# Optimization experiments

Hardware: AMD Instinct MI355X
Metric: run time of the kernel (lower is better)

The kernel has to match this reference:

```python
import jax, jax.numpy as jnp
import numpy as np

SPECIES = (0, 1)
CUTOFF = 6.0
N_ATOMS, N_EDGES, N_TRIPLETS = 20000, 500000, 2000000

G2_ETAS = np.array([0.003214, 0.035711, 0.071421, 0.124987, 0.214264, 0.357106, 0.714213, 1.428426], dtype=np.float32)
G4_ETAS = np.array([0.000357, 0.028569, 0.089277], dtype=np.float32)
G4_ZETAS = np.array([1.0, 2.0, 4.0], dtype=np.float32)
G4_LMDAS = np.array([-1.0, 1.0], dtype=np.float32)


def setup_inputs() -> dict:
    key = jax.random.key(0)
    ks = jax.random.split(key, 6)
    atomic_numbers = jax.random.randint(ks[0], (N_ATOMS,), 0, 2, dtype=jnp.int32)
    edge_index = jax.random.randint(ks[1], (2, N_EDGES), 0, N_ATOMS, dtype=jnp.int32)
    D_st = jax.random.uniform(ks[2], (N_EDGES,), minval=0.5, maxval=6.5, dtype=jnp.float32)
    id3_ba = jax.random.randint(ks[3], (N_TRIPLETS,), 0, N_EDGES, dtype=jnp.int32)
    id3_ca = jax.random.randint(ks[4], (N_TRIPLETS,), 0, N_EDGES, dtype=jnp.int32)
    cosphi = jax.random.uniform(ks[5], (N_TRIPLETS,), minval=-1.0, maxval=1.0, dtype=jnp.float32)
    # per-key parameters: 4 ordered species pairs for G2, 6 species triples for G4
    g2_etas = jnp.tile(jnp.asarray(G2_ETAS), (4, 1))
    g4_etas = jnp.tile(jnp.asarray(G4_ETAS), (6, 1))
    g4_zetas = jnp.tile(jnp.asarray(G4_ZETAS), (6, 1))
    g4_lmdas = jnp.tile(jnp.asarray(G4_LMDAS), (6, 1))
    return {"atomic_numbers": atomic_numbers, "edge_index": edge_index, "D_st": D_st,
            "id3_ba": id3_ba, "id3_ca": id3_ca, "cosphi": cosphi,
            "g2_etas": g2_etas, "g4_etas": g4_etas, "g4_zetas": g4_zetas, "g4_lmdas": g4_lmdas}


def _fc(R):
    # cosine cutoff (no in-range bool here; G4 applies its own range masks)
    return 0.5 * jnp.cos(jnp.pi * R / CUTOFF) + 0.5


def _acsf(atomic_numbers, edge_index, D_st, id3_ba, id3_ca, cosphi,
          g2_etas, g4_etas, g4_zetas, g4_lmdas):
    N = atomic_numbers.shape[0]
    dt = D_st.dtype
    src, tgt = edge_index[0], edge_index[1]
    an_src, an_tgt = atomic_numbers[src], atomic_numbers[tgt]

    # ---- triplet geometry (masking replaces boolean gather; scatter-add is equivalent) ----
    m3 = id3_ba > id3_ca                       # [T] triplet dedup mask
    R_ba = D_st[id3_ba]                        # [T]
    R_ca = D_st[id3_ca]
    sb = atomic_numbers[src[id3_ba]]           # species of edge-ba source
    tb = atomic_numbers[tgt[id3_ba]]           # species of central atom a
    sc = atomic_numbers[src[id3_ca]]
    seg3 = tgt[id3_ba]                         # scatter target: central atom index
    Rbc2 = R_ba * R_ba + R_ca * R_ca - 2.0 * R_ba * R_ca * cosphi
    R_bc = jnp.sqrt(jnp.maximum(Rbc2, 1e-12))
    in_range = ((R_bc < CUTOFF) & (R_ba < CUTOFF) & (R_ca < CUTOFF)).astype(dt)
    cut3 = _fc(R_ca) * _fc(R_bc) * _fc(R_ba) * in_range   # [T]
    r2sum = R_bc * R_bc + R_ba * R_ba + R_ca * R_ca       # [T]

    # ---- G2: per (source, target) species pair ----
    cut2 = _fc(D_st)                           # [E]
    d2 = D_st * D_st
    g2_per = {}
    k = 0
    for a1 in SPECIES:
        for a2 in SPECIES:
            w = ((an_tgt == a2) & (an_src == a1)).astype(dt)       # [E]
            res = (cut2 * w)[:, None] * jnp.exp(-g2_etas[k][None, :] * d2[:, None])  # [E,8]
            g2_per[(a1, a2)] = jax.ops.segment_sum(res, tgt, num_segments=N)        # [N,8]
            k += 1

    # ---- G4: per (a, b, c) species triple (b<=c) ----
    ns = len(SPECIES)
    g4_per = {}
    k = 0
    for a in SPECIES:
        for i in range(ns):
            b = SPECIES[i]
            for j in range(i, ns):
                c = SPECIES[j]
                idx = (((sb == b) & (tb == a) & (sc == c)) |
                       ((sb == c) & (tb == a) & (sc == b)))
                w = (m3 & idx).astype(dt)                                  # [T]
                eta, zta, lmda = g4_etas[k], g4_zetas[k], g4_lmdas[k]
                rad = jnp.exp(-eta[None, :] * r2sum[:, None])              # [T,3]
                cl = jnp.abs(1.0 + lmda[None, :, None] * cosphi[:, None, None]) ** zta[None, None, :]  # [T,2,3]
                res = cl[:, None, :, :] * rad[:, :, None, None] * (cut3 * w)[:, None, None, None]      # [T,3,2,3]
                g4 = jax.ops.segment_sum(res, seg3, num_segments=N)        # [N,3,2,3]
                g4_per[(a, b, c)] = (2.0 ** (1.0 - zta))[None, None, None, :] * g4
                k += 1

    # ---- assemble per-atom descriptor [N, 70]; rows carry their species' descriptor ----
    outs = []
    for a in SPECIES:
        mask = (atomic_numbers == a).astype(dt)[:, None]
        g2s = jnp.stack([g2_per[(s, a)] for s in SPECIES], axis=-1).reshape(N, -1)   # [N,16]
        trips = [(b, c) for i, b in enumerate(SPECIES) for c in SPECIES[i:]]
        g4s = jnp.stack([g4_per[(a, b, c)] for (b, c) in trips], axis=-1).reshape(N, -1)  # [N,54]
        outs.append(mask * jnp.concatenate([g2s, g4s], axis=-1))
    return outs[0] + outs[1]


def reference(atomic_numbers, edge_index, D_st, id3_ba, id3_ca, cosphi,
              g2_etas, g4_etas, g4_zetas, g4_lmdas):
    return _acsf(atomic_numbers, edge_index, D_st, id3_ba, id3_ca, cosphi,
                 g2_etas, g4_etas, g4_zetas, g4_lmdas)
```

## Files before the change

kernel.cpp:

```cpp
#include <hip/hip_runtime.h>


#define CAP_T 96
#define CAP_E 64

static __device__ __forceinline__ float fc_dev(float R) {
    const float PI_OVER_CUT = 0.52359877559829887308f;
    return fmaf(0.5f, __cosf(PI_OVER_CUT * R), 0.5f);
}


__global__ void edges_bin_kernel(const int* __restrict__ an,
                                 const int* __restrict__ ei,
                                 const float* __restrict__ D,
                                 const float* __restrict__ g2_etas,
                                 uint2* __restrict__ epack,
                                 int* __restrict__ ecount,
                                 float2* __restrict__ erec,
                                 float* __restrict__ out, int E) {
    int e = blockIdx.x * blockDim.x + threadIdx.x;
    if (e >= E) return;
    float d = D[e];
    int src = ei[e];
    int tgt = ei[E + e];
    int as = an[src];
    epack[e] = make_uint2(__float_as_uint(d), ((unsigned)tgt << 1) | (unsigned)as);
    float fcv = fc_dev(d);
    float d2 = d * d;
    int slot = atomicAdd(&ecount[tgt], 1);
    if (slot < CAP_E) {
        unsigned fp = (__float_as_uint(fcv) & ~1u) | (unsigned)as;
        erec[(size_t)tgt * CAP_E + slot] = make_float2(__uint_as_float(fp), d2);
    } else {
        int at = an[tgt];
        const float* eta = g2_etas + (as * 2 + at) * 8;
        float* row = out + (size_t)tgt * 70 + as;
#pragma unroll
        for (int i = 0; i < 8; ++i)
            atomicAdd(row + 2 * i, fcv * __expf(-eta[i] * d2));
    }
}

static __device__ __forceinline__ void process_triplet(
        int eba, int eca, float cph,
        const uint2* __restrict__ epack,
        const int* __restrict__ an,
        const float* __restrict__ g4_etas,
        const float* __restrict__ g4_zetas,
        const float* __restrict__ g4_lmdas,
        int* __restrict__ tcount, float4* __restrict__ trec,
        float* __restrict__ out) {
    if (eba <= eca) return;
    uint2 pb = epack[eba];
    uint2 pc = epack[eca];
    float R_ba = __uint_as_float(pb.x);
    float R_ca = __uint_as_float(pc.x);
    if (R_ba >= 6.0f || R_ca >= 6.0f) return;
    float Rbc2 = R_ba * R_ba + R_ca * R_ca - 2.0f * R_ba * R_ca * cph;
    float Rm2 = fmaxf(Rbc2, 1e-12f);
    float R_bc = sqrtf(Rm2);
    if (R_bc >= 6.0f) return;
    int seg = (int)(pb.y >> 1);
    int trip = (int)(pb.y & 1u) + (int)(pc.y & 1u);
    float cut3 = fc_dev(R_ba) * fc_dev(R_ca) * fc_dev(R_bc);
    float r2sum = Rm2 + R_ba * R_ba + R_ca * R_ca;
    float lg0 = __log2f(fabsf(fmaf(-1.0f, cph, 1.0f)));
    float lg1 = __log2f(fabsf(fmaf(+1.0f, cph, 1.0f)));
    int slot = atomicAdd(&tcount[seg], 1);
    if (slot < CAP_T) {
        unsigned cu = (__float_as_uint(cut3) & ~3u) | (unsigned)trip;
        trec[(size_t)seg * CAP_T + slot] =
            make_float4(__uint_as_float(cu), r2sum, lg0, lg1);
    } else {
        int A = an[seg];
        int k4 = A * 3 + trip;
        const float* eta = g4_etas + k4 * 3;
        const float* zet = g4_zetas + k4 * 3;
        const float* lmd = g4_lmdas + k4 * 2;
        float rad[3];
#pragma unroll
        for (int e2 = 0; e2 < 3; ++e2)
            rad[e2] = __expf(-eta[e2] * r2sum) * cut3;
        float l0 = (lmd[0] < 0.0f) ? lg0 : lg1;
        float l1 = (lmd[1] < 0.0f) ? lg0 : lg1;
        float* row = out + (size_t)seg * 70 + 16 + trip;
#pragma unroll
        for (int z = 0; z < 3; ++z) {
            float zv = zet[z], base = 1.0f - zv;
            float c0 = exp2f(fmaf(zv, l0, base));
            float c1 = exp2f(fmaf(zv, l1, base));
#pragma unroll
            for (int e2 = 0; e2 < 3; ++e2) {
                atomicAdd(row + ((e2 * 2 + 0) * 3 + z) * 3, c0 * rad[e2]);
                atomicAdd(row + ((e2 * 2 + 1) * 3 + z) * 3, c1 * rad[e2]);
            }
        }
    }
}

__global__ void trip_bin_kernel(const uint2* __restrict__ epack,
                                const int* __restrict__ id3_ba,
                                const int* __restrict__ id3_ca,
                                const float* __restrict__ cosphi,
                                const int* __restrict__ an,
                                const float* __restrict__ g4_etas,
                                const float* __restrict__ g4_zetas,
                                const float* __restrict__ g4_lmdas,
                                int* __restrict__ tcount,
                                float4* __restrict__ trec,
                                float* __restrict__ out, int T) {
    int i = blockIdx.x * blockDim.x + threadIdx.x;
    int t0 = i * 2;
    if (t0 >= T) return;
    if (t0 + 1 < T) {
        int2   ba = ((const int2*)id3_ba)[i];
        int2   ca = ((const int2*)id3_ca)[i];
        float2 cp = ((const float2*)cosphi)[i];
        process_triplet(ba.x, ca.x, cp.x, epack, an, g4_etas, g4_zetas,
                        g4_lmdas, tcount, trec, out);
        process_triplet(ba.y, ca.y, cp.y, epack, an, g4_etas, g4_zetas,
                        g4_lmdas, tcount, trec, out);
    } else {
        process_triplet(id3_ba[t0], id3_ca[t0], cosphi[t0], epack, an,
                        g4_etas, g4_zetas, g4_lmdas, tcount, trec, out);
    }
}

__global__ __launch_bounds__(256) void gather_kernel(
        const int* __restrict__ an,
        const float* __restrict__ g2_etas,
        const float* __restrict__ g4_etas,
        const float* __restrict__ g4_zetas,
        const float* __restrict__ g4_lmdas,
        const int* __restrict__ tcount, const float4* __restrict__ trec,
        const int* __restrict__ ecount, const float2* __restrict__ erec,
        float* __restrict__ out, int N) {
    __shared__ float4 sg4[4][64];
    __shared__ float2 sg2[4][64];
    int w = threadIdx.x >> 6;
    int lane = threadIdx.x & 63;
    int a = blockIdx.x * 4 + w;
    if (a >= N) return;
    int A = an[a];

    int trip_c = lane % 3;
    int z_c = (lane / 3) % 3;
    int l_c = (lane / 9) % 2;
    int e_c = lane / 18;
    float eta = 0.f, zv = 0.f, base = 1.f;
    if (lane < 54) {
        int k4 = A * 3 + trip_c;
        eta = g4_etas[k4 * 3 + e_c];
        zv  = g4_zetas[k4 * 3 + z_c];
        float lm = g4_lmdas[k4 * 2 + l_c];
        l_c = (lm < 0.0f) ? 0 : 1;
        base = 1.0f - zv;
    }
    int n_t = min(tcount[a], CAP_T);
    const float4* rec = trec + (size_t)a * CAP_T;
    float acc = 0.0f;
    for (int b0 = 0; b0 < n_t; b0 += 64) {
        int nch = min(64, n_t - b0);
        if (lane < nch) sg4[w][lane] = rec[b0 + lane];
        for (int i = 0; i < nch; ++i) {
            float4 b = sg4[w][i];
            unsigned cu = __float_as_uint(b.x);
            int btr = (int)(cu & 3u);
            float bc = __uint_as_float(cu & ~3u);
            float radv = __expf(-eta * b.y);
            float lg = l_c ? b.w : b.z;
            float cl = exp2f(fmaf(zv, lg, base));
            acc += (btr == trip_c) ? cl * radv * bc : 0.0f;
        }
    }
    if (lane < 54) out[(size_t)a * 70 + 16 + lane] += acc;

    int s_c = lane & 1;
    int i_c = lane >> 1;
    float eta2 = (lane < 16) ? g2_etas[(s_c * 2 + A) * 8 + i_c] : 0.0f;
    int n_e = min(ecount[a], CAP_E);
    const float2* erc = erec + (size_t)a * CAP_E;
    float acc2 = 0.0f;
    for (int b0 = 0; b0 < n_e; b0 += 64) {
        int nch = min(64, n_e - b0);
        if (lane < nch) sg2[w][lane] = erc[b0 + lane];
        for (int i = 0; i < nch; ++i) {
            float2 b = sg2[w][i];
            unsigned fp = __float_as_uint(b.x);
            int sp = (int)(fp & 1u);
            float fcv = __uint_as_float(fp & ~1u);
            float v = fcv * __expf(-eta2 * b.y);
            acc2 += (sp == s_c) ? v : 0.0f;
        }
    }
    if (lane < 16) out[(size_t)a * 70 + lane] += acc2;
}


__global__ void acsf_edges_kernel(const int* __restrict__ an,
                                  const int* __restrict__ ei,
                                  const float* __restrict__ D,
                                  const float* __restrict__ g2_etas,
                                  float2* __restrict__ edata,
                                  float* __restrict__ out,
                                  int E, int use_ws) {
    int e = blockIdx.x * blockDim.x + threadIdx.x;
    if (e >= E) return;
    float d = D[e];
    float cut2 = fc_dev(d);
    if (use_ws) edata[e] = make_float2(d, cut2);
    int src = ei[e];
    int tgt = ei[E + e];
    int as = an[src];
    int at = an[tgt];
    float d2 = d * d;
    const float* eta = g2_etas + (as * 2 + at) * 8;
    float* row = out + (size_t)tgt * 70 + as;
#pragma unroll
    for (int i = 0; i < 8; ++i)
        atomicAdd(row + 2 * i, cut2 * __expf(-eta[i] * d2));
}

__global__ void acsf_triplets_kernel(const int* __restrict__ an,
                                     const int* __restrict__ ei,
                                     const float* __restrict__ D,
                                     const float2* __restrict__ edata,
                                     const int* __restrict__ id3_ba,
                                     const int* __restrict__ id3_ca,
                                     const float* __restrict__ cosphi,
                                     const float* __restrict__ g4_etas,
                                     const float* __restrict__ g4_zetas,
                                     const float* __restrict__ g4_lmdas,
                                     float* __restrict__ out,
                                     int T, int E, int use_ws) {
    int t = blockIdx.x * blockDim.x + threadIdx.x;
    if (t >= T) return;
    int eba = id3_ba[t];
    int eca = id3_ca[t];
    if (eba <= eca) return;
    float R_ba, R_ca, fba, fca;
    if (use_ws) {
        float2 va = edata[eba];
        float2 vb = edata[eca];
        R_ba = va.x; fba = va.y;
        R_ca = vb.x; fca = vb.y;
    } else {
        R_ba = D[eba]; R_ca = D[eca];
        fba = fc_dev(R_ba); fca = fc_dev(R_ca);
    }
    if (R_ba >= 6.0f || R_ca >= 6.0f) return;
    float cph = cosphi[t];
    float Rbc2 = R_ba * R_ba + R_ca * R_ca - 2.0f * R_ba * R_ca * cph;
    float Rm2 = fmaxf(Rbc2, 1e-12f);
    float R_bc = sqrtf(Rm2);
    if (R_bc >= 6.0f) return;
    int seg = ei[E + eba];
    int A = an[seg];
    int sb = an[ei[eba]];
    int sc = an[ei[eca]];
    int trip = sb + sc;
    int k4 = A * 3 + trip;
    float cut3 = fba * fca * fc_dev(R_bc);
    float r2sum = Rm2 + R_ba * R_ba + R_ca * R_ca;
    const float* eta = g4_etas + k4 * 3;
    const float* zet = g4_zetas + k4 * 3;
    const float* lmd = g4_lmdas + k4 * 2;
    float rad[3];
#pragma unroll
    for (int e2 = 0; e2 < 3; ++e2)
        rad[e2] = __expf(-eta[e2] * r2sum) * cut3;
    float lg0 = __log2f(fabsf(fmaf(lmd[0], cph, 1.0f)));
    float lg1 = __log2f(fabsf(fmaf(lmd[1], cph, 1.0f)));
    float* row = out + (size_t)seg * 70 + 16 + trip;
#pragma unroll
    for (int z = 0; z < 3; ++z) {
        float zv = zet[z], bse = 1.0f - zv;
        float c0 = exp2f(fmaf(zv, lg0, bse));
        float c1 = exp2f(fmaf(zv, lg1, bse));
#pragma unroll
        for (int e2 = 0; e2 < 3; ++e2) {
            atomicAdd(row + ((e2 * 2 + 0) * 3 + z) * 3, c0 * rad[e2]);
            atomicAdd(row + ((e2 * 2 + 1) * 3 + z) * 3, c1 * rad[e2]);
        }
    }
}


extern "C" void kernel_launch(void* const* d_in, const int* in_sizes, int n_in,
                              void* d_out, int out_size, void* d_ws, size_t ws_size,
                              hipStream_t stream) {
    const int*   an       = (const int*)d_in[0];
    const int*   ei       = (const int*)d_in[1];
    const float* D        = (const float*)d_in[2];
    const int*   id3_ba   = (const int*)d_in[3];
    const int*   id3_ca   = (const int*)d_in[4];
    const float* cosphi   = (const float*)d_in[5];
    const float* g2_etas  = (const float*)d_in[6];
    const float* g4_etas  = (const float*)d_in[7];
    const float* g4_zetas = (const float*)d_in[8];
    const float* g4_lmdas = (const float*)d_in[9];
    (void)n_in;

    int N = in_sizes[0];
    int E = in_sizes[2];
    int T = in_sizes[3];
    float* out = (float*)d_out;

    size_t trec_b  = (size_t)N * CAP_T * sizeof(float4);
    size_t epack_b = (size_t)E * sizeof(uint2);
    size_t erec_b  = (size_t)N * CAP_E * sizeof(float2);
    size_t cnt_b   = (size_t)N * sizeof(int) * 2;
    size_t need = trec_b + epack_b + erec_b + cnt_b;

    const int blk = 256;
    hipMemsetAsync(d_out, 0, (size_t)out_size * sizeof(float), stream);

    if (ws_size >= need) {
        char* p = (char*)d_ws;
        float4* trec  = (float4*)p;            p += trec_b;
        uint2*  epack = (uint2*)p;             p += epack_b;
        float2* erec  = (float2*)p;            p += erec_b;
        int*    tcount = (int*)p;
        int*    ecount = tcount + N;
        hipMemsetAsync(tcount, 0, cnt_b, stream);

        edges_bin_kernel<<<(E + blk - 1) / blk, blk, 0, stream>>>(
            an, ei, D, g2_etas, epack, ecount, erec, out, E);
        int tthreads = (T + 1) / 2;
        trip_bin_kernel<<<(tthreads + blk - 1) / blk, blk, 0, stream>>>(
            epack, id3_ba, id3_ca, cosphi, an,
            g4_etas, g4_zetas, g4_lmdas, tcount, trec, out, T);
        gather_kernel<<<(N + 3) / 4, blk, 0, stream>>>(
            an, g2_etas, g4_etas, g4_zetas, g4_lmdas,
            tcount, trec, ecount, erec, out, N);
    } else {
        int use_ws = (ws_size >= (size_t)E * sizeof(float2)) ? 1 : 0;
        float2* edata = (float2*)d_ws;
        acsf_edges_kernel<<<(E + blk - 1) / blk, blk, 0, stream>>>(
            an, ei, D, g2_etas, edata, out, E, use_ws);
        acsf_triplets_kernel<<<(T + blk - 1) / blk, blk, 0, stream>>>(
            an, ei, D, edata, id3_ba, id3_ca, cosphi,
            g4_etas, g4_zetas, g4_lmdas, out, T, E, use_ws);
    }
}
```

Measured before the change: 196.1 us.

## Quantize edge and triplet records to shrink intermediate traffic

Edge data is packed into one 32-bit word (a 16-bit quantized distance, the target index and the source species), and triplet records shrink from float4 to float2 by quantizing cosphi and the cutoff product. The gather kernel now recomputes the log terms and fc from the decoded values. Triplet and edge binning each handle more items per thread with vector nontemporal loads. This cuts memory traffic and atomic-bin storage, but adds quantization error, extra transcendental work in the gather, and a limit of N <= 32767.

```diff
diff --git a/kernel.cpp b/kernel.cpp
--- a/kernel.cpp
+++ b/kernel.cpp
@@ -3,74 +3,99 @@
 
 #define CAP_T 96
 #define CAP_E 64
+
+typedef int    vi2 __attribute__((ext_vector_type(2)));
+typedef int    vi4 __attribute__((ext_vector_type(4)));
+typedef float  vf2 __attribute__((ext_vector_type(2)));
+typedef float  vf4 __attribute__((ext_vector_type(4)));
 
 static __device__ __forceinline__ float fc_dev(float R) {
     const float PI_OVER_CUT = 0.52359877559829887308f;
     return fmaf(0.5f, __cosf(PI_OVER_CUT * R), 0.5f);
 }
 
+static __device__ __forceinline__ unsigned enc_R(float d) {
+    float u = rintf(d * (65535.0f / 8.0f));
+    u = fminf(fmaxf(u, 0.0f), 65535.0f);
+    return (unsigned)u;
+}
+static __device__ __forceinline__ float dec_R(unsigned pk) {
+    return (float)(pk >> 16) * (8.0f / 65535.0f);
+}
+
+
+static __device__ __forceinline__ void process_edge(
+        int e, float d, int src, int tgt,
+        const int* __restrict__ an, const float* __restrict__ g2_etas,
+        unsigned* __restrict__ epack, int* __restrict__ ecount,
+        unsigned* __restrict__ erec, float* __restrict__ out) {
+    int as = an[src];
+    unsigned pk = (enc_R(d) << 16) | ((unsigned)tgt << 1) | (unsigned)as;
+    epack[e] = pk;
+    int slot = atomicAdd(&ecount[tgt], 1);
+    if (slot < CAP_E) {
+        erec[(size_t)tgt * CAP_E + slot] = pk;
+    } else {
+        float fcv = fc_dev(d), d2 = d * d;
+        int at = an[tgt];
+        const float* eta = g2_etas + (as * 2 + at) * 8;
+        float* row = out + (size_t)tgt * 70 + as;
+#pragma unroll
+        for (int i = 0; i < 8; ++i)
+            atomicAdd(row + 2 * i, fcv * __expf(-eta[i] * d2));
+    }
+}
 
 __global__ void edges_bin_kernel(const int* __restrict__ an,
                                  const int* __restrict__ ei,
                                  const float* __restrict__ D,
                                  const float* __restrict__ g2_etas,
-                                 uint2* __restrict__ epack,
+                                 unsigned* __restrict__ epack,
                                  int* __restrict__ ecount,
-                                 float2* __restrict__ erec,
+                                 unsigned* __restrict__ erec,
                                  float* __restrict__ out, int E) {
-    int e = blockIdx.x * blockDim.x + threadIdx.x;
-    if (e >= E) return;
-    float d = D[e];
-    int src = ei[e];
-    int tgt = ei[E + e];
-    int as = an[src];
-    epack[e] = make_uint2(__float_as_uint(d), ((unsigned)tgt << 1) | (unsigned)as);
-    float fcv = fc_dev(d);
-    float d2 = d * d;
-    int slot = atomicAdd(&ecount[tgt], 1);
-    if (slot < CAP_E) {
-        unsigned fp = (__float_as_uint(fcv) & ~1u) | (unsigned)as;
-        erec[(size_t)tgt * CAP_E + slot] = make_float2(__uint_as_float(fp), d2);
-    } else {
-        int at = an[tgt];
-        const float* eta = g2_etas + (as * 2 + at) * 8;
-        float* row = out + (size_t)tgt * 70 + as;
-#pragma unroll
-        for (int i = 0; i < 8; ++i)
-            atomicAdd(row + 2 * i, fcv * __expf(-eta[i] * d2));
+    int i = blockIdx.x * blockDim.x + threadIdx.x;
+    int e0 = i * 2;
+    if (e0 >= E) return;
+    if (e0 + 1 < E) {
+        vi2 sp = __builtin_nontemporal_load((const vi2*)ei + i);
+        vi2 tp = __builtin_nontemporal_load((const vi2*)(ei + E) + i);
+        vf2 dp = __builtin_nontemporal_load((const vf2*)D + i);
+        process_edge(e0,     dp.x, sp.x, tp.x, an, g2_etas, epack, ecount, erec, out);
+        process_edge(e0 + 1, dp.y, sp.y, tp.y, an, g2_etas, epack, ecount, erec, out);
+    } else {
+        process_edge(e0, D[e0], ei[e0], ei[E + e0], an, g2_etas, epack, ecount,
+                     erec, out);
     }
 }
 
 static __device__ __forceinline__ void process_triplet(
-        int eba, int eca, float cph,
-        const uint2* __restrict__ epack,
+        unsigned pb, unsigned pc, float cph,
         const int* __restrict__ an,
         const float* __restrict__ g4_etas,
         const float* __restrict__ g4_zetas,
         const float* __restrict__ g4_lmdas,
-        int* __restrict__ tcount, float4* __restrict__ trec,
+        int* __restrict__ tcount, vf2* __restrict__ trec,
         float* __restrict__ out) {
-    if (eba <= eca) return;
-    uint2 pb = epack[eba];
-    uint2 pc = epack[eca];
-    float R_ba = __uint_as_float(pb.x);
-    float R_ca = __uint_as_float(pc.x);
+    float R_ba = dec_R(pb);
+    float R_ca = dec_R(pc);
     if (R_ba >= 6.0f || R_ca >= 6.0f) return;
     float Rbc2 = R_ba * R_ba + R_ca * R_ca - 2.0f * R_ba * R_ca * cph;
     float Rm2 = fmaxf(Rbc2, 1e-12f);
     float R_bc = sqrtf(Rm2);
     if (R_bc >= 6.0f) return;
-    int seg = (int)(pb.y >> 1);
-    int trip = (int)(pb.y & 1u) + (int)(pc.y & 1u);
+    int seg = (int)((pb >> 1) & 0x7FFFu);
+    int trip = (int)(pb & 1u) + (int)(pc & 1u);
     float cut3 = fc_dev(R_ba) * fc_dev(R_ca) * fc_dev(R_bc);
     float r2sum = Rm2 + R_ba * R_ba + R_ca * R_ca;
-    float lg0 = __log2f(fabsf(fmaf(-1.0f, cph, 1.0f)));
-    float lg1 = __log2f(fabsf(fmaf(+1.0f, cph, 1.0f)));
     int slot = atomicAdd(&tcount[seg], 1);
     if (slot < CAP_T) {
-        unsigned cu = (__float_as_uint(cut3) & ~3u) | (unsigned)trip;
-        trec[(size_t)seg * CAP_T + slot] =
-            make_float4(__uint_as_float(cu), r2sum, lg0, lg1);
+        float cqf = fminf(fmaxf(fmaf(cph, 32767.5f, 32767.5f), 0.0f), 65535.0f);
+        unsigned cq = (unsigned)rintf(cqf);
+        unsigned c3q = (unsigned)rintf(cut3 * 16383.0f);
+        unsigned w0 = (cq << 16) | (c3q << 2) | (unsigned)trip;
+        vf2 r; r.x = __uint_as_float(w0); r.y = r2sum;
+        trec[(size_t)seg * CAP_T + slot] = r;
     } else {
         int A = an[seg];
         int k4 = A * 3 + trip;
@@ -81,14 +106,14 @@
 #pragma unroll
         for (int e2 = 0; e2 < 3; ++e2)
             rad[e2] = __expf(-eta[e2] * r2sum) * cut3;
-        float l0 = (lmd[0] < 0.0f) ? lg0 : lg1;
-        float l1 = (lmd[1] < 0.0f) ? lg0 : lg1;
+        float lg0 = __log2f(fabsf(fmaf(lmd[0], cph, 1.0f)));
+        float lg1 = __log2f(fabsf(fmaf(lmd[1], cph, 1.0f)));
         float* row = out + (size_t)seg * 70 + 16 + trip;
 #pragma unroll
         for (int z = 0; z < 3; ++z) {
             float zv = zet[z], base = 1.0f - zv;
-            float c0 = exp2f(fmaf(zv, l0, base));
-            float c1 = exp2f(fmaf(zv, l1, base));
+            float c0 = exp2f(fmaf(zv, lg0, base));
+            float c1 = exp2f(fmaf(zv, lg1, base));
 #pragma unroll
             for (int e2 = 0; e2 < 3; ++e2) {
                 atomicAdd(row + ((e2 * 2 + 0) * 3 + z) * 3, c0 * rad[e2]);
@@ -98,7 +123,7 @@
     }
 }
 
-__global__ void trip_bin_kernel(const uint2* __restrict__ epack,
+__global__ void trip_bin_kernel(const unsigned* __restrict__ epack,
                                 const int* __restrict__ id3_ba,
                                 const int* __restrict__ id3_ca,
                                 const float* __restrict__ cosphi,
@@ -107,22 +132,45 @@
                                 const float* __restrict__ g4_zetas,
                                 const float* __restrict__ g4_lmdas,
                                 int* __restrict__ tcount,
-                                float4* __restrict__ trec,
+                                vf2* __restrict__ trec,
                                 float* __restrict__ out, int T) {
     int i = blockIdx.x * blockDim.x + threadIdx.x;
-    int t0 = i * 2;
+    int t0 = i * 4;
     if (t0 >= T) return;
-    if (t0 + 1 < T) {
-        int2   ba = ((const int2*)id3_ba)[i];
-        int2   ca = ((const int2*)id3_ca)[i];
-        float2 cp = ((const float2*)cosphi)[i];
-        process_triplet(ba.x, ca.x, cp.x, epack, an, g4_etas, g4_zetas,
-                        g4_lmdas, tcount, trec, out);
-        process_triplet(ba.y, ca.y, cp.y, epack, an, g4_etas, g4_zetas,
-                        g4_lmdas, tcount, trec, out);
-    } else {
-        process_triplet(id3_ba[t0], id3_ca[t0], cosphi[t0], epack, an,
-                        g4_etas, g4_zetas, g4_lmdas, tcount, trec, out);
+    int ba[4], ca[4];
+    float cp[4];
+    if (t0 + 3 < T) {
+        vi4 b4 = __builtin_nontemporal_load((const vi4*)id3_ba + i);
+        vi4 c4 = __builtin_nontemporal_load((const vi4*)id3_ca + i);
+        vf4 p4 = __builtin_nontemporal_load((const vf4*)cosphi + i);
+        ba[0] = b4.x; ba[1] = b4.y; ba[2] = b4.z; ba[3] = b4.w;
+        ca[0] = c4.x; ca[1] = c4.y; ca[2] = c4.z; ca[3] = c4.w;
+        cp[0] = p4.x; cp[1] = p4.y; cp[2] = p4.z; cp[3] = p4.w;
+    } else {
+#pragma unroll
+        for (int k = 0; k < 4; ++k) {
+            int t = t0 + k;
+            ba[k] = (t < T) ? id3_ba[t] : 0;
+            ca[k] = (t < T) ? id3_ca[t] : 0;
+            cp[k] = (t < T) ? cosphi[t] : 0.0f;
+        }
+    }
+    unsigned pb[4], pc[4];
+    bool m[4];
+#pragma unroll
+    for (int k = 0; k < 4; ++k) {
+        m[k] = ba[k] > ca[k];
+        pb[k] = 0u; pc[k] = 0u;
+        if (m[k]) {
+            pb[k] = epack[ba[k]];
+            pc[k] = epack[ca[k]];
+        }
+    }
+#pragma unroll
+    for (int k = 0; k < 4; ++k) {
+        if (m[k])
+            process_triplet(pb[k], pc[k], cp[k], an, g4_etas, g4_zetas,
+                            g4_lmdas, tcount, trec, out);
     }
 }
 
@@ -132,11 +180,11 @@
         const float* __restrict__ g4_etas,
         const float* __restrict__ g4_zetas,
         const float* __restrict__ g4_lmdas,
-        const int* __restrict__ tcount, const float4* __restrict__ trec,
-        const int* __restrict__ ecount, const float2* __restrict__ erec,
+        const int* __restrict__ tcount, const vf2* __restrict__ trec,
+        const int* __restrict__ ecount, const unsigned* __restrict__ erec,
         float* __restrict__ out, int N) {
-    __shared__ float4 sg4[4][64];
-    __shared__ float2 sg2[4][64];
+    __shared__ vf2      sg4[4][64];
+    __shared__ unsigned sg2[4][64];
     int w = threadIdx.x >> 6;
     int lane = threadIdx.x & 63;
     int a = blockIdx.x * 4 + w;
@@ -147,30 +195,30 @@
     int z_c = (lane / 3) % 3;
     int l_c = (lane / 9) % 2;
     int e_c = lane / 18;
-    float eta = 0.f, zv = 0.f, base = 1.f;
+    float eta = 0.f, zv = 0.f, lm = 0.f, base = 1.f;
     if (lane < 54) {
         int k4 = A * 3 + trip_c;
         eta = g4_etas[k4 * 3 + e_c];
         zv  = g4_zetas[k4 * 3 + z_c];
-        float lm = g4_lmdas[k4 * 2 + l_c];
-        l_c = (lm < 0.0f) ? 0 : 1;
+        lm  = g4_lmdas[k4 * 2 + l_c];
         base = 1.0f - zv;
     }
     int n_t = min(tcount[a], CAP_T);
-    const float4* rec = trec + (size_t)a * CAP_T;
+    const vf2* rec = trec + (size_t)a * CAP_T;
     float acc = 0.0f;
     for (int b0 = 0; b0 < n_t; b0 += 64) {
         int nch = min(64, n_t - b0);
-        if (lane < nch) sg4[w][lane] = rec[b0 + lane];
+        if (lane < nch) sg4[w][lane] = __builtin_nontemporal_load(rec + b0 + lane);
         for (int i = 0; i < nch; ++i) {
-            float4 b = sg4[w][i];
-            unsigned cu = __float_as_uint(b.x);
-            int btr = (int)(cu & 3u);
-            float bc = __uint_as_float(cu & ~3u);
+            vf2 b = sg4[w][i];
+            unsigned w0 = __float_as_uint(b.x);
+            int btr = (int)(w0 & 3u);
+            float cut3 = (float)((w0 >> 2) & 0x3FFFu) * (1.0f / 16383.0f);
+            float c = fmaf((float)(w0 >> 16), 2.0f / 65535.0f, -1.0f);
             float radv = __expf(-eta * b.y);
-            float lg = l_c ? b.w : b.z;
-            float cl = exp2f(fmaf(zv, lg, base));
-            acc += (btr == trip_c) ? cl * radv * bc : 0.0f;
+            float al = fabsf(fmaf(lm, c, 1.0f));
+            float cl = exp2f(fmaf(zv, __log2f(al), base));
+            acc += (btr == trip_c) ? cl * radv * cut3 : 0.0f;
         }
     }
     if (lane < 54) out[(size_t)a * 70 + 16 + lane] += acc;
@@ -179,17 +227,16 @@
     int i_c = lane >> 1;
     float eta2 = (lane < 16) ? g2_etas[(s_c * 2 + A) * 8 + i_c] : 0.0f;
     int n_e = min(ecount[a], CAP_E);
-    const float2* erc = erec + (size_t)a * CAP_E;
+    const unsigned* erc = erec + (size_t)a * CAP_E;
     float acc2 = 0.0f;
     for (int b0 = 0; b0 < n_e; b0 += 64) {
         int nch = min(64, n_e - b0);
-        if (lane < nch) sg2[w][lane] = erc[b0 + lane];
+        if (lane < nch) sg2[w][lane] = __builtin_nontemporal_load(erc + b0 + lane);
         for (int i = 0; i < nch; ++i) {
-            float2 b = sg2[w][i];
-            unsigned fp = __float_as_uint(b.x);
-            int sp = (int)(fp & 1u);
-            float fcv = __uint_as_float(fp & ~1u);
-            float v = fcv * __expf(-eta2 * b.y);
+            unsigned pk = sg2[w][i];
+            int sp = (int)(pk & 1u);
+            float d = dec_R(pk);
+            float v = fc_dev(d) * __expf(-eta2 * d * d);
             acc2 += (sp == s_c) ? v : 0.0f;
         }
     }
@@ -306,27 +353,28 @@
     int T = in_sizes[3];
     float* out = (float*)d_out;
 
-    size_t trec_b  = (size_t)N * CAP_T * sizeof(float4);
-    size_t epack_b = (size_t)E * sizeof(uint2);
-    size_t erec_b  = (size_t)N * CAP_E * sizeof(float2);
+    size_t trec_b  = (size_t)N * CAP_T * sizeof(vf2);
+    size_t epack_b = (size_t)((E + 1) & ~1) * sizeof(unsigned);
+    size_t erec_b  = (size_t)N * CAP_E * sizeof(unsigned);
     size_t cnt_b   = (size_t)N * sizeof(int) * 2;
     size_t need = trec_b + epack_b + erec_b + cnt_b;
 
     const int blk = 256;
-    hipMemsetAsync(d_out, 0, (size_t)out_size * sizeof(float), stream);
-
-    if (ws_size >= need) {
+    (void)hipMemsetAsync(d_out, 0, (size_t)out_size * sizeof(float), stream);
+
+    if (ws_size >= need && N <= 32767) {
         char* p = (char*)d_ws;
-        float4* trec  = (float4*)p;            p += trec_b;
-        uint2*  epack = (uint2*)p;             p += epack_b;
-        float2* erec  = (float2*)p;            p += erec_b;
-        int*    tcount = (int*)p;
-        int*    ecount = tcount + N;
-        hipMemsetAsync(tcount, 0, cnt_b, stream);
-
-        edges_bin_kernel<<<(E + blk - 1) / blk, blk, 0, stream>>>(
+        vf2*      trec  = (vf2*)p;             p += trec_b;
+        unsigned* epack = (unsigned*)p;        p += epack_b;
+        unsigned* erec  = (unsigned*)p;        p += erec_b;
+        int*      tcount = (int*)p;
+        int*      ecount = tcount + N;
+        (void)hipMemsetAsync(tcount, 0, cnt_b, stream);
+
+        int ethreads = (E + 1) / 2;
+        edges_bin_kernel<<<(ethreads + blk - 1) / blk, blk, 0, stream>>>(
             an, ei, D, g2_etas, epack, ecount, erec, out, E);
-        int tthreads = (T + 1) / 2;
+        int tthreads = (T + 3) / 4;
         trip_bin_kernel<<<(tthreads + blk - 1) / blk, blk, 0, stream>>>(
             epack, id3_ba, id3_ca, cosphi, an,
             g4_etas, g4_zetas, g4_lmdas, tcount, trec, out, T);
```

Result: slower. 209.3 us (+6.7%).
